# Performance work log

Hardware: AMD Instinct MI355X
Metric: run time of the kernel (lower is better)

Reference implementation:

```python
import jax, jax.numpy as jnp
import numpy as np

C = 1.0          # ball curvature (k = -1/c with c=1.0 in the torch module)
SQC = 1.0        # sqrt(C)
LN_EPS = 1e-5

def _artanh(x):
    return jnp.arctanh(jnp.clip(x, -1.0 + 1e-7, 1.0 - 1e-7))

def _norm(x):
    # last-dim L2 norm, clamped away from zero for stable division
    return jnp.clip(jnp.sqrt(jnp.sum(x * x, axis=-1, keepdims=True)), 1e-7, None)

def expmap0(u):
    un = _norm(u)
    return jnp.tanh(SQC * un) * u / (SQC * un)

def logmap0(y):
    yn = _norm(y)
    return _artanh(SQC * yn) * y / (SQC * yn)

def mobius_add(x, y):
    x2 = jnp.sum(x * x, axis=-1, keepdims=True)
    y2 = jnp.sum(y * y, axis=-1, keepdims=True)
    xy = jnp.sum(x * y, axis=-1, keepdims=True)
    num = (1.0 + 2.0 * C * xy + C * y2) * x + (1.0 - C * x2) * y
    den = 1.0 + 2.0 * C * xy + C * C * x2 * y2
    return num / jnp.clip(den, 1e-15, None)

def mobius_matvec(W, x):
    # W: [H, D], x: [B, D] -> [B, H]
    mx = x @ W.T
    xn = _norm(x)
    mxn = _norm(mx)
    res = jnp.tanh(mxn / xn * _artanh(SQC * xn)) * mx / (SQC * mxn)
    return jnp.where(mxn <= 1e-7, jnp.zeros_like(res), res)

def mobius_pointwise_mul(w, x):
    wx = w * x
    xn = _norm(x)
    wxn = _norm(wx)
    res = jnp.tanh(wxn / xn * _artanh(SQC * xn)) * wx / (SQC * wxn)
    return jnp.where(wxn <= 1e-7, jnp.zeros_like(res), res)

def layer_norm(x, g, b):
    mu = jnp.mean(x, axis=-1, keepdims=True)
    var = jnp.mean((x - mu) ** 2, axis=-1, keepdims=True)
    return (x - mu) * jax.lax.rsqrt(var + LN_EPS) * g + b

def one_rnn_transform(W, h, U, x, b):
    Wh = mobius_matvec(W, h)
    Ux = mobius_matvec(U, x)
    return mobius_add(mobius_add(Wh, Ux), b)

def setup_inputs() -> dict:
    key = jax.random.key(0)
    B, I, H = 65536, 256, 256
    k1, k2, k3, k4, k5 = jax.random.split(key, 5)
    stdv = 1.0 / np.sqrt(H)
    # points on the Poincare ball via expmap0 of small tangent vectors
    x = expmap0(0.02 * jax.random.normal(k1, (B, I), dtype=jnp.float32))
    hx = expmap0(0.02 * jax.random.normal(k2, (B, H), dtype=jnp.float32))
    weight_ih = jax.random.uniform(k3, (3 * H, I), dtype=jnp.float32, minval=-stdv, maxval=stdv)
    weight_hh = jax.random.uniform(k4, (3 * H, H), dtype=jnp.float32, minval=-stdv, maxval=stdv)
    bias = 0.01 * jax.random.normal(k5, (3, H), dtype=jnp.float32)
    ln_gamma = jnp.ones((3, H), dtype=jnp.float32)
    ln_beta = jnp.zeros((3, H), dtype=jnp.float32)
    return {"input": x, "hx": hx, "weight_ih": weight_ih, "weight_hh": weight_hh,
            "bias": bias, "ln_gamma": ln_gamma, "ln_beta": ln_beta}

def reference(input, hx, weight_ih, weight_hh, bias, ln_gamma, ln_beta):
    H = hx.shape[-1]
    W_ir, W_ih_, W_iz = weight_ih[:H], weight_ih[H:2*H], weight_ih[2*H:]
    W_hr, W_hh_, W_hz = weight_hh[:H], weight_hh[H:2*H], weight_hh[2*H:]
    b_r, b_h, b_z = bias[0], bias[1], bias[2]
    temp_z = logmap0(one_rnn_transform(W_hz, hx, W_iz, input, b_z))
    temp_r = logmap0(one_rnn_transform(W_hr, hx, W_ir, input, b_r))
    z_t = jax.nn.sigmoid(layer_norm(temp_z, ln_gamma[0], ln_beta[0]))
    r_t = jax.nn.sigmoid(layer_norm(temp_r, ln_gamma[1], ln_beta[1]))
    rh_t = mobius_pointwise_mul(r_t, hx)
    h_tilde = one_rnn_transform(W_hh_, rh_t, W_ih_, input, b_h)
    h_tilde = expmap0(jnp.tanh(layer_norm(logmap0(h_tilde), ln_gamma[2], ln_beta[2])))
    temp_1 = mobius_pointwise_mul(1.0 - z_t, hx)
    temp_2 = mobius_pointwise_mul(z_t, h_tilde)
    return mobius_add(temp_1, temp_2)
```

## Files before the change

kernel.cpp:

```cpp
#include <hip/hip_runtime.h>
#include <math.h>

#define HD  256
#define BM  16
#define NTH 256

typedef __attribute__((ext_vector_type(8))) short bf16x8;
typedef __attribute__((ext_vector_type(4))) float f32x4;

__device__ __forceinline__ float rcp_f(float x){ return __builtin_amdgcn_rcpf(x); }
__device__ __forceinline__ float tanh_f(float x){
  float ax = fabsf(x);
  float e  = __expf(-2.f*ax);
  float t  = (1.f - e) * rcp_f(1.f + e);
  return copysignf(t, x);
}
__device__ __forceinline__ float artanh_f(float v){
  v = fminf(fmaxf(v, -1.f + 1e-7f), 1.f - 1e-7f);
  return 0.5f * __logf((1.f + v) * rcp_f(1.f - v));
}
__device__ __forceinline__ float sigmoid_f(float v){ return rcp_f(1.f + __expf(-v)); }
__device__ __forceinline__ unsigned short f2bf(float f){
  unsigned u = __float_as_uint(f);
  u += 0x7FFFu + ((u >> 16) & 1u);
  return (unsigned short)(u >> 16);
}
__device__ __forceinline__ float bf2f(unsigned short h){
  return __uint_as_float(((unsigned)h) << 16);
}
__device__ __forceinline__ int swz(int R, int C){
  return R*HD + (((C >> 3) ^ (R & 7)) << 3) + (C & 7);
}

__global__ void convert_w_kernel(const float* __restrict__ Wih,
                                 const float* __restrict__ Whh,
                                 unsigned short* __restrict__ wb){
  int c = blockIdx.x * blockDim.x + threadIdx.x;
  if (c >= 6 * 8192) return;
  int mat = c >> 13;
  int ci  = c & 8191;
  int l = ci & 63, st = ci >> 6;
  int s = st & 7, ct = st >> 3;
  int col = ct * 16 + (l & 15);
  int k0  = s * 32 + (l >> 4) * 8;
  const float* src = (mat < 3) ? (Wih + (size_t)mat * HD * HD)
                               : (Whh + (size_t)(mat - 3) * HD * HD);
  const float* p = src + (size_t)col * HD + k0;
  unsigned short tmp[8];
  #pragma unroll
  for (int j = 0; j < 8; ++j) tmp[j] = f2bf(p[j]);
  *(bf16x8*)(wb + (size_t)mat * 65536 + (size_t)ci * 8) = *(bf16x8*)tmp;
}

__device__ __forceinline__ void reduce7(
    const f32x4* A, const f32x4* B, const float* bt,
    float (*RED)[33], int wc, int lr, int lg){
  float p[7][4];
  #pragma unroll
  for (int q = 0; q < 4; ++q){
    float a2=0.f,b2=0.f,ab=0.f,sA=0.f,sB=0.f,Ab=0.f,Bb=0.f;
    #pragma unroll
    for (int n = 0; n < 4; ++n){
      float ae = A[n][q], be = B[n][q], bv = bt[n];
      a2 = fmaf(ae,ae,a2); b2 = fmaf(be,be,b2); ab = fmaf(ae,be,ab);
      sA += ae; sB += be; Ab = fmaf(ae,bv,Ab); Bb = fmaf(be,bv,Bb);
    }
    p[0][q]=a2; p[1][q]=b2; p[2][q]=ab; p[3][q]=sA; p[4][q]=sB; p[5][q]=Ab; p[6][q]=Bb;
  }
  #pragma unroll
  for (int j = 0; j < 7; ++j)
    #pragma unroll
    for (int q = 0; q < 4; ++q){
      float v = p[j][q];
      v += __shfl_xor(v,1); v += __shfl_xor(v,2);
      v += __shfl_xor(v,4); v += __shfl_xor(v,8);
      p[j][q] = v;
    }
  if (lr == 0){
    #pragma unroll
    for (int q = 0; q < 4; ++q){
      int R = lg*4 + q;
      #pragma unroll
      for (int j = 0; j < 7; ++j) RED[R][wc*8 + j] = p[j][q];
    }
  }
}

__device__ __forceinline__ void chain5(
    const float* s, float bb, float sbs,
    float an, float aa, float bn, float ba, float* o){
  float mraw = sqrtf(s[0]); float mA = fmaxf(mraw, 1e-7f);
  float tA = tanh_f(mA / an * aa);
  float sa  = (mraw <= 1e-7f) ? 0.f : tA / mA;
  float x2a = (mraw <= 1e-7f) ? 0.f : tA*tA;
  float nraw = sqrtf(s[1]); float mB = fmaxf(nraw, 1e-7f);
  float tB = tanh_f(mB / bn * ba);
  float sb_ = (nraw <= 1e-7f) ? 0.f : tB / mB;
  float x2b = (nraw <= 1e-7f) ? 0.f : tB*tB;
  float xy = sa*sb_*s[2];
  float ca = 1.f + 2.f*xy + x2b;
  float cb = 1.f - x2a;
  float den = fmaxf(1.f + 2.f*xy + x2a*x2b, 1e-15f);
  float u = ca*sa/den, v = cb*sb_/den;
  float P2 = u*u*s[0] + 2.f*u*v*s[2] + v*v*s[1];
  float Pb = u*s[5] + v*s[6];
  float sP = u*s[3] + v*s[4];
  float ca2 = 1.f + 2.f*Pb + bb;
  float cb2 = 1.f - P2;
  float den2 = fmaxf(1.f + 2.f*Pb + P2*bb, 1e-15f);
  float pp = ca2/den2, ww = cb2/den2;
  float Q2 = pp*pp*P2 + 2.f*pp*ww*Pb + ww*ww*bb;
  float sQsum = pp*sP + ww*sbs;
  float qn = fmaxf(sqrtf(Q2), 1e-7f);
  float sQ = artanh_f(qn) / qn;
  float mu = sQ*sQsum*(1.f/HD);
  float e2 = sQ*sQ*Q2*(1.f/HD);
  float is = rsqrtf(e2 - mu*mu + 1e-5f);
  o[0] = sQ*pp*u;  o[1] = sQ*pp*v;  o[2] = sQ*ww;
  o[3] = mu;       o[4] = is;
}

__global__ __launch_bounds__(NTH, 2) void mobius_gru_mfma(
    const float* __restrict__ x, const float* __restrict__ hx,
    const unsigned short* __restrict__ wbih, const unsigned short* __restrict__ wbhh,
    const float* __restrict__ bias, const float* __restrict__ gam,
    const float* __restrict__ bet, float* __restrict__ out, int B){
  __shared__ unsigned short xb[BM*HD];
  __shared__ unsigned short hb[BM*HD];
  __shared__ float REDZ[BM][33];
  __shared__ float REDR[BM][33];
  __shared__ float kco[BM][10];
  __shared__ float srow[8][BM];
  __shared__ float sbb[8];

  const int t  = threadIdx.x;
  const int l  = t & 63;
  const int lr = l & 15, lg = l >> 4;
  const int wc = t >> 6;
  const size_t row0 = (size_t)blockIdx.x * BM;

  {
    float* spart = &REDZ[0][0];
    int r = t >> 4, seg = t & 15;
    const float* xp = x  + (row0 + r)*HD + seg*16;
    const float* hp = hx + (row0 + r)*HD + seg*16;
    float sx = 0.f, sh = 0.f;
    #pragma unroll
    for (int i = 0; i < 4; ++i){
      int c = seg*16 + i*4;
      int di = swz(r, c);
      float4 v = *(const float4*)(xp + i*4);
      sx += v.x*v.x + v.y*v.y + v.z*v.z + v.w*v.w;
      ushort4 o = { f2bf(v.x), f2bf(v.y), f2bf(v.z), f2bf(v.w) };
      *(ushort4*)&xb[di] = o;
      v = *(const float4*)(hp + i*4);
      sh += v.x*v.x + v.y*v.y + v.z*v.z + v.w*v.w;
      ushort4 o2 = { f2bf(v.x), f2bf(v.y), f2bf(v.z), f2bf(v.w) };
      *(ushort4*)&hb[di] = o2;
    }
    spart[r*16 + seg] = sx; spart[256 + r*16 + seg] = sh;
  }
  if (t >= 64 && t < 256){
    int g = (t >> 6) - 1;
    float4 b4 = *(const float4*)&bias[g*HD + (t & 63)*4];
    float p2 = b4.x*b4.x + b4.y*b4.y + b4.z*b4.z + b4.w*b4.w;
    float ps = b4.x + b4.y + b4.z + b4.w;
    #pragma unroll
    for (int m = 1; m <= 32; m <<= 1){ p2 += __shfl_xor(p2, m); ps += __shfl_xor(ps, m); }
    if ((t & 63) == 0){ sbb[g] = p2; sbb[4+g] = ps; }
  }
  __syncthreads();
  if (t < BM){
    float* spart = &REDZ[0][0];
    float sx = 0.f, sh = 0.f;
    #pragma unroll
    for (int i = 0; i < 16; ++i){ sx += spart[t*16 + i]; sh += spart[256 + t*16 + i]; }
    float xn = fmaxf(sqrtf(sx), 1e-7f);
    float hn = fmaxf(sqrtf(sh), 1e-7f);
    srow[0][t] = xn; srow[1][t] = artanh_f(xn);
    srow[2][t] = hn; srow[3][t] = artanh_f(hn);
  }
  __syncthreads();

  f32x4 Az[4], Bz[4], Ar[4], Br[4], Bh[4];
  float btz[4], btr[4];
  #pragma unroll
  for (int n = 0; n < 4; ++n){
    int C = wc*64 + n*16 + lr;
    btz[n] = bias[2*HD + C];
    btr[n] = bias[C];
    Az[n] = (f32x4){0.f,0.f,0.f,0.f}; Bz[n] = (f32x4){0.f,0.f,0.f,0.f};
    Ar[n] = (f32x4){0.f,0.f,0.f,0.f}; Br[n] = (f32x4){0.f,0.f,0.f,0.f};
    Bh[n] = (f32x4){0.f,0.f,0.f,0.f};
  }
  {
    const unsigned short* wHz = wbhh + 2*65536;
    const unsigned short* wXz = wbih + 2*65536;
    const unsigned short* wHr = wbhh;
    const unsigned short* wXr = wbih;
    const unsigned short* wXh = wbih + 65536;
    #pragma unroll
    for (int s = 0; s < 8; ++s){
      int idx = lr*HD + (((4*s + lg) ^ (lr & 7)) << 3);
      bf16x8 ah = *(const bf16x8*)&hb[idx];
      bf16x8 ax = *(const bf16x8*)&xb[idx];
      #pragma unroll
      for (int n = 0; n < 4; ++n){
        int off = (((wc*4 + n)*8 + s)*64 + l)*8;
        bf16x8 bhz = *(const bf16x8*)(wHz + off);
        bf16x8 bxz = *(const bf16x8*)(wXz + off);
        bf16x8 bhr = *(const bf16x8*)(wHr + off);
        bf16x8 bxr = *(const bf16x8*)(wXr + off);
        bf16x8 bxh = *(const bf16x8*)(wXh + off);
        Az[n] = __builtin_amdgcn_mfma_f32_16x16x32_bf16(ah, bhz, Az[n], 0, 0, 0);
        Bz[n] = __builtin_amdgcn_mfma_f32_16x16x32_bf16(ax, bxz, Bz[n], 0, 0, 0);
        Ar[n] = __builtin_amdgcn_mfma_f32_16x16x32_bf16(ah, bhr, Ar[n], 0, 0, 0);
        Br[n] = __builtin_amdgcn_mfma_f32_16x16x32_bf16(ax, bxr, Br[n], 0, 0, 0);
        Bh[n] = __builtin_amdgcn_mfma_f32_16x16x32_bf16(ax, bxh, Bh[n], 0, 0, 0);
      }
    }
  }
  reduce7(Az, Bz, btz, REDZ, wc, lr, lg);
  reduce7(Ar, Br, btr, REDR, wc, lr, lg);
  __syncthreads();
  if (t < 32){
    int R = t & 15, gsel = t >> 4;
    float (*REDp)[33] = gsel ? REDR : REDZ;
    int gidx = gsel ? 0 : 2;
    float s[7];
    #pragma unroll
    for (int j = 0; j < 7; ++j)
      s[j] = REDp[R][j] + REDp[R][8+j] + REDp[R][16+j] + REDp[R][24+j];
    float o[5];
    chain5(s, sbb[gidx], sbb[4+gidx],
           srow[2][R], srow[3][R], srow[0][R], srow[1][R], o);
    #pragma unroll
    for (int k = 0; k < 5; ++k) kco[R][gsel*5 + k] = o[k];
  }
  __syncthreads();

  unsigned ztp[4][2];
  float hvreg[4][4];
  {
    float gvz[4], bvz[4], gvr[4], bvr[4];
    #pragma unroll
    for (int n = 0; n < 4; ++n){
      int C = wc*64 + n*16 + lr;
      gvz[n] = gam[C];      bvz[n] = bet[C];
      gvr[n] = gam[HD + C]; bvr[n] = bet[HD + C];
    }
    #pragma unroll
    for (int q = 0; q < 4; ++q){
      int R = lg*4 + q;
      float KAz=kco[R][0], KBz=kco[R][1], Kbz=kco[R][2], muz=kco[R][3], isz=kco[R][4];
      float KAr=kco[R][5], KBr=kco[R][6], Kbr=kco[R][7], mur=kco[R][8], isr=kco[R][9];
      float acc = 0.f;
      #pragma unroll
      for (int n = 0; n < 4; ++n){
        int C = wc*64 + n*16 + lr;
        float hv = bf2f(hb[swz(R, C)]);
        hvreg[n][q] = hv;
        float lnz = (KAz*Az[n][q] + KBz*Bz[n][q] + Kbz*btz[n] - muz)*isz*gvz[n] + bvz[n];
        unsigned zb = f2bf(sigmoid_f(lnz));
        if ((q & 1) == 0) ztp[n][q>>1] = zb;
        else              ztp[n][q>>1] |= (zb << 16);
        float lnr = (KAr*Ar[n][q] + KBr*Br[n][q] + Kbr*btr[n] - mur)*isr*gvr[n] + bvr[n];
        float rhv = sigmoid_f(lnr) * hv;
        Br[n][q] = rhv;
        acc = fmaf(rhv, rhv, acc);
      }
      float v2 = acc;
      v2 += __shfl_xor(v2,1); v2 += __shfl_xor(v2,2);
      v2 += __shfl_xor(v2,4); v2 += __shfl_xor(v2,8);
      if (lr == 0) REDZ[R][wc*8] = v2;
    }
  }
  __syncthreads();
  if (t < BM){
    int R = t;
    float s0 = REDZ[R][0] + REDZ[R][8] + REDZ[R][16] + REDZ[R][24];
    float wraw = sqrtf(s0); float wn = fmaxf(wraw, 1e-7f);
    float s = tanh_f(wn / srow[2][R] * srow[3][R]);
    float sc = (wraw <= 1e-7f) ? 0.f : s / wn;
    float rn = fmaxf((wraw <= 1e-7f) ? 0.f : fabsf(s), 1e-7f);
    kco[R][0] = sc; srow[4][R] = rn; srow[5][R] = artanh_f(rn);
  }
  __syncthreads();
  #pragma unroll
  for (int q = 0; q < 4; ++q){
    int R = lg*4 + q;
    float sc = kco[R][0];
    #pragma unroll
    for (int n = 0; n < 4; ++n){
      int C = wc*64 + n*16 + lr;
      hb[swz(R, C)] = f2bf(sc * Br[n][q]);
    }
  }
  __syncthreads();

  f32x4 Ah[4];
  float bth[4];
  #pragma unroll
  for (int n = 0; n < 4; ++n){
    int C = wc*64 + n*16 + lr;
    bth[n] = bias[HD + C];
    Ah[n] = (f32x4){0.f,0.f,0.f,0.f};
  }
  {
    const unsigned short* wHh = wbhh + 65536;
    #pragma unroll
    for (int s = 0; s < 8; ++s){
      int idx = lr*HD + (((4*s + lg) ^ (lr & 7)) << 3);
      bf16x8 ar = *(const bf16x8*)&hb[idx];
      #pragma unroll
      for (int n = 0; n < 4; ++n){
        int off = (((wc*4 + n)*8 + s)*64 + l)*8;
        bf16x8 bh = *(const bf16x8*)(wHh + off);
        Ah[n] = __builtin_amdgcn_mfma_f32_16x16x32_bf16(ar, bh, Ah[n], 0, 0, 0);
      }
    }
  }
  reduce7(Ah, Bh, bth, REDZ, wc, lr, lg);
  __syncthreads();
  if (t < BM){
    int R = t;
    float s[7];
    #pragma unroll
    for (int j = 0; j < 7; ++j)
      s[j] = REDZ[R][j] + REDZ[R][8+j] + REDZ[R][16+j] + REDZ[R][24+j];
    float o[5];
    chain5(s, sbb[1], sbb[5],
           srow[4][R], srow[5][R], srow[0][R], srow[1][R], o);
    #pragma unroll
    for (int k = 0; k < 5; ++k) kco[R][k] = o[k];
  }
  __syncthreads();
  {
    float gvh[4], bvh[4];
    #pragma unroll
    for (int n = 0; n < 4; ++n){
      int C = wc*64 + n*16 + lr;
      gvh[n] = gam[2*HD + C]; bvh[n] = bet[2*HD + C];
    }
    #pragma unroll
    for (int q = 0; q < 4; ++q){
      int R = lg*4 + q;
      float KA=kco[R][0], KB=kco[R][1], Kb=kco[R][2], mu=kco[R][3], is=kco[R][4];
      float acc = 0.f;
      #pragma unroll
      for (int n = 0; n < 4; ++n){
        float ln = (KA*Ah[n][q] + KB*Bh[n][q] + Kb*bth[n] - mu)*is*gvh[n] + bvh[n];
        float uv = tanh_f(ln);
        Ah[n][q] = uv;
        acc = fmaf(uv, uv, acc);
      }
      float v2 = acc;
      v2 += __shfl_xor(v2,1); v2 += __shfl_xor(v2,2);
      v2 += __shfl_xor(v2,4); v2 += __shfl_xor(v2,8);
      if (lr == 0) REDZ[R][wc*8] = v2;
    }
  }
  __syncthreads();
  if (t < BM){
    int R = t;
    float s0 = REDZ[R][0] + REDZ[R][8] + REDZ[R][16] + REDZ[R][24];
    float unraw = sqrtf(s0);
    float un = fmaxf(unraw, 1e-7f);
    float es = tanh_f(un) / un;
    float htn = fmaxf(es * unraw, 1e-7f);
    kco[R][0] = es; srow[6][R] = htn; srow[7][R] = artanh_f(htn);
  }
  __syncthreads();

  #pragma unroll
  for (int q = 0; q < 4; ++q){
    int R = lg*4 + q;
    float es = kco[R][0];
    float a1 = 0.f, a2 = 0.f, a12 = 0.f;
    #pragma unroll
    for (int n = 0; n < 4; ++n){
      unsigned zp = ztp[n][q >> 1];
      float zv = __uint_as_float((q & 1) ? (zp & 0xFFFF0000u) : (zp << 16));
      float w2v = zv * es * Ah[n][q];
      float w1v = (1.f - zv) * hvreg[n][q];
      Ah[n][q] = w2v;
      Bh[n][q] = w1v;
      a1 = fmaf(w1v, w1v, a1); a2 = fmaf(w2v, w2v, a2); a12 = fmaf(w1v, w2v, a12);
    }
    float v1 = a1, v2 = a2, v3 = a12;
    v1 += __shfl_xor(v1,1); v2 += __shfl_xor(v2,1); v3 += __shfl_xor(v3,1);
    v1 += __shfl_xor(v1,2); v2 += __shfl_xor(v2,2); v3 += __shfl_xor(v3,2);
    v1 += __shfl_xor(v1,4); v2 += __shfl_xor(v2,4); v3 += __shfl_xor(v3,4);
    v1 += __shfl_xor(v1,8); v2 += __shfl_xor(v2,8); v3 += __shfl_xor(v3,8);
    if (lr == 0){
      REDZ[R][wc*8]   = v1;
      REDZ[R][wc*8+1] = v2;
      REDZ[R][wc*8+2] = v3;
    }
  }
  __syncthreads();
  if (t < BM){
    int R = t;
    float s1  = REDZ[R][0] + REDZ[R][8]  + REDZ[R][16] + REDZ[R][24];
    float s2  = REDZ[R][1] + REDZ[R][9]  + REDZ[R][17] + REDZ[R][25];
    float s12 = REDZ[R][2] + REDZ[R][10] + REDZ[R][18] + REDZ[R][26];
    float raw1 = sqrtf(s1); float n1 = fmaxf(raw1, 1e-7f);
    float ss1 = tanh_f(n1 / srow[2][R] * srow[3][R]);
    float sc1 = (raw1 <= 1e-7f) ? 0.f : ss1 / n1;
    float t1  = (raw1 <= 1e-7f) ? 0.f : ss1*ss1;
    float raw2 = sqrtf(s2); float n2 = fmaxf(raw2, 1e-7f);
    float ss2 = tanh_f(n2 / srow[6][R] * srow[7][R]);
    float sc2 = (raw2 <= 1e-7f) ? 0.f : ss2 / n2;
    float t2  = (raw2 <= 1e-7f) ? 0.f : ss2*ss2;
    float xy = sc1*sc2*s12;
    float ca = 1.f + 2.f*xy + t2;
    float cb = 1.f - t1;
    float den = fmaxf(1.f + 2.f*xy + t1*t2, 1e-15f);
    kco[R][0] = ca*sc1/den;
    kco[R][1] = cb*sc2/den;
  }
  __syncthreads();
  #pragma unroll
  for (int q = 0; q < 4; ++q){
    int R = lg*4 + q;
    float cw1 = kco[R][0], cw2 = kco[R][1];
    #pragma unroll
    for (int n = 0; n < 4; ++n){
      int C = wc*64 + n*16 + lr;
      out[(row0 + R)*HD + C] = cw1*Bh[n][q] + cw2*Ah[n][q];
    }
  }
}

extern "C" void kernel_launch(void* const* d_in, const int* in_sizes, int n_in,
                              void* d_out, int out_size, void* d_ws, size_t ws_size,
                              hipStream_t stream){
  const float* x    = (const float*)d_in[0];
  const float* hx   = (const float*)d_in[1];
  const float* Wih  = (const float*)d_in[2];
  const float* Whh  = (const float*)d_in[3];
  const float* bias = (const float*)d_in[4];
  const float* gam  = (const float*)d_in[5];
  const float* bet  = (const float*)d_in[6];
  float* out = (float*)d_out;
  unsigned short* wb = (unsigned short*)d_ws;
  const int B = in_sizes[0] / HD;

  hipLaunchKernelGGL(convert_w_kernel, dim3(192), dim3(256), 0, stream, Wih, Whh, wb);
  hipLaunchKernelGGL(mobius_gru_mfma, dim3(B / BM), dim3(NTH), 0, stream,
                     x, hx, wb, wb + 3*65536, bias, gam, bet, out, B);
}
```

Baseline: 219.1 us.

## Replace single-thread row epilogues with redundant per-wave compute and shuffles

Per-row scalar coefficient stages that ran on 16-32 threads, wrote to shared memory and needed an extra barrier each are now computed redundantly by every wave. Values reach the needed lanes by cross-lane shuffles, which removes several __syncthreads and the kco shared array. Reduction partials move to spare column slots so they do not collide with live data. The cost is duplicated transcendental math in every wave and more shuffle traffic.

```diff
diff --git a/kernel.cpp b/kernel.cpp
--- a/kernel.cpp
+++ b/kernel.cpp
@@ -129,7 +129,6 @@
   __shared__ unsigned short hb[BM*HD];
   __shared__ float REDZ[BM][33];
   __shared__ float REDR[BM][33];
-  __shared__ float kco[BM][10];
   __shared__ float srow[8][BM];
   __shared__ float sbb[8];
 
@@ -137,6 +136,7 @@
   const int l  = t & 63;
   const int lr = l & 15, lg = l >> 4;
   const int wc = t >> 6;
+  const int crow = lg*4 + (lr & 3);
   const size_t row0 = (size_t)blockIdx.x * BM;
 
   {
@@ -170,15 +170,15 @@
     if ((t & 63) == 0){ sbb[g] = p2; sbb[4+g] = ps; }
   }
   __syncthreads();
-  if (t < BM){
+  if (t < 32){
     float* spart = &REDZ[0][0];
-    float sx = 0.f, sh = 0.f;
-    #pragma unroll
-    for (int i = 0; i < 16; ++i){ sx += spart[t*16 + i]; sh += spart[256 + t*16 + i]; }
-    float xn = fmaxf(sqrtf(sx), 1e-7f);
-    float hn = fmaxf(sqrtf(sh), 1e-7f);
-    srow[0][t] = xn; srow[1][t] = artanh_f(xn);
-    srow[2][t] = hn; srow[3][t] = artanh_f(hn);
+    int R = t & 15, sel = t >> 4;
+    const float* base = spart + sel*256;
+    float sv = 0.f;
+    #pragma unroll
+    for (int i = 0; i < 16; ++i) sv += base[R*16 + i];
+    float nn = fmaxf(sqrtf(sv), 1e-7f);
+    srow[sel*2][R] = nn; srow[sel*2+1][R] = artanh_f(nn);
   }
   __syncthreads();
 
@@ -223,21 +223,29 @@
   reduce7(Az, Bz, btz, REDZ, wc, lr, lg);
   reduce7(Ar, Br, btr, REDR, wc, lr, lg);
   __syncthreads();
-  if (t < 32){
-    int R = t & 15, gsel = t >> 4;
-    float (*REDp)[33] = gsel ? REDR : REDZ;
-    int gidx = gsel ? 0 : 2;
+
+  float KAz[4],KBz[4],Kbz[4],muz[4],isz[4];
+  float KAr[4],KBr[4],Kbr[4],mur[4],ISr[4];
+  {
+    bool doR = (lr >= 8);
+    float (*REDp)[33] = doR ? REDR : REDZ;
+    int gidx = doR ? 0 : 2;
     float s[7];
     #pragma unroll
     for (int j = 0; j < 7; ++j)
-      s[j] = REDp[R][j] + REDp[R][8+j] + REDp[R][16+j] + REDp[R][24+j];
+      s[j] = REDp[crow][j] + REDp[crow][8+j] + REDp[crow][16+j] + REDp[crow][24+j];
     float o[5];
     chain5(s, sbb[gidx], sbb[4+gidx],
-           srow[2][R], srow[3][R], srow[0][R], srow[1][R], o);
-    #pragma unroll
-    for (int k = 0; k < 5; ++k) kco[R][gsel*5 + k] = o[k];
-  }
-  __syncthreads();
+           srow[2][crow], srow[3][crow], srow[0][crow], srow[1][crow], o);
+    #pragma unroll
+    for (int q = 0; q < 4; ++q){
+      int zs = (l & 48) + q, rs = zs + 8;
+      KAz[q]=__shfl(o[0],zs); KBz[q]=__shfl(o[1],zs); Kbz[q]=__shfl(o[2],zs);
+      muz[q]=__shfl(o[3],zs); isz[q]=__shfl(o[4],zs);
+      KAr[q]=__shfl(o[0],rs); KBr[q]=__shfl(o[1],rs); Kbr[q]=__shfl(o[2],rs);
+      mur[q]=__shfl(o[3],rs); ISr[q]=__shfl(o[4],rs);
+    }
+  }
 
   unsigned ztp[4][2];
   float hvreg[4][4];
@@ -252,19 +260,17 @@
     #pragma unroll
     for (int q = 0; q < 4; ++q){
       int R = lg*4 + q;
-      float KAz=kco[R][0], KBz=kco[R][1], Kbz=kco[R][2], muz=kco[R][3], isz=kco[R][4];
-      float KAr=kco[R][5], KBr=kco[R][6], Kbr=kco[R][7], mur=kco[R][8], isr=kco[R][9];
       float acc = 0.f;
       #pragma unroll
       for (int n = 0; n < 4; ++n){
         int C = wc*64 + n*16 + lr;
         float hv = bf2f(hb[swz(R, C)]);
         hvreg[n][q] = hv;
-        float lnz = (KAz*Az[n][q] + KBz*Bz[n][q] + Kbz*btz[n] - muz)*isz*gvz[n] + bvz[n];
+        float lnz = (KAz[q]*Az[n][q] + KBz[q]*Bz[n][q] + Kbz[q]*btz[n] - muz[q])*isz[q]*gvz[n] + bvz[n];
         unsigned zb = f2bf(sigmoid_f(lnz));
         if ((q & 1) == 0) ztp[n][q>>1] = zb;
         else              ztp[n][q>>1] |= (zb << 16);
-        float lnr = (KAr*Ar[n][q] + KBr*Br[n][q] + Kbr*btr[n] - mur)*isr*gvr[n] + bvr[n];
+        float lnr = (KAr[q]*Ar[n][q] + KBr[q]*Br[n][q] + Kbr[q]*btr[n] - mur[q])*ISr[q]*gvr[n] + bvr[n];
         float rhv = sigmoid_f(lnr) * hv;
         Br[n][q] = rhv;
         acc = fmaf(rhv, rhv, acc);
@@ -272,28 +278,29 @@
       float v2 = acc;
       v2 += __shfl_xor(v2,1); v2 += __shfl_xor(v2,2);
       v2 += __shfl_xor(v2,4); v2 += __shfl_xor(v2,8);
-      if (lr == 0) REDZ[R][wc*8] = v2;
-    }
-  }
-  __syncthreads();
-  if (t < BM){
-    int R = t;
-    float s0 = REDZ[R][0] + REDZ[R][8] + REDZ[R][16] + REDZ[R][24];
+      if (lr == 0) REDZ[R][wc*8 + 7] = v2;
+    }
+  }
+  __syncthreads();
+
+  float scq[4];
+  {
+    float s0 = REDZ[crow][7] + REDZ[crow][15] + REDZ[crow][23] + REDZ[crow][31];
     float wraw = sqrtf(s0); float wn = fmaxf(wraw, 1e-7f);
-    float s = tanh_f(wn / srow[2][R] * srow[3][R]);
-    float sc = (wraw <= 1e-7f) ? 0.f : s / wn;
-    float rn = fmaxf((wraw <= 1e-7f) ? 0.f : fabsf(s), 1e-7f);
-    kco[R][0] = sc; srow[4][R] = rn; srow[5][R] = artanh_f(rn);
-  }
-  __syncthreads();
+    float sv = tanh_f(wn / srow[2][crow] * srow[3][crow]);
+    float sc = (wraw <= 1e-7f) ? 0.f : sv / wn;
+    float rn = fmaxf((wraw <= 1e-7f) ? 0.f : fabsf(sv), 1e-7f);
+    if (wc == 0 && lr < 4){ srow[4][crow] = rn; srow[5][crow] = artanh_f(rn); }
+    #pragma unroll
+    for (int q = 0; q < 4; ++q) scq[q] = __shfl(sc, (l & 48) + q);
+  }
   #pragma unroll
   for (int q = 0; q < 4; ++q){
     int R = lg*4 + q;
-    float sc = kco[R][0];
     #pragma unroll
     for (int n = 0; n < 4; ++n){
       int C = wc*64 + n*16 + lr;
-      hb[swz(R, C)] = f2bf(sc * Br[n][q]);
+      hb[swz(R, C)] = f2bf(scq[q] * Br[n][q]);
     }
   }
   __syncthreads();
@@ -322,19 +329,23 @@
   }
   reduce7(Ah, Bh, bth, REDZ, wc, lr, lg);
   __syncthreads();
-  if (t < BM){
-    int R = t;
+
+  float KA[4],KB[4],Kb[4],MU[4],IS[4];
+  {
     float s[7];
     #pragma unroll
     for (int j = 0; j < 7; ++j)
-      s[j] = REDZ[R][j] + REDZ[R][8+j] + REDZ[R][16+j] + REDZ[R][24+j];
+      s[j] = REDZ[crow][j] + REDZ[crow][8+j] + REDZ[crow][16+j] + REDZ[crow][24+j];
     float o[5];
     chain5(s, sbb[1], sbb[5],
-           srow[4][R], srow[5][R], srow[0][R], srow[1][R], o);
-    #pragma unroll
-    for (int k = 0; k < 5; ++k) kco[R][k] = o[k];
-  }
-  __syncthreads();
+           srow[4][crow], srow[5][crow], srow[0][crow], srow[1][crow], o);
+    #pragma unroll
+    for (int q = 0; q < 4; ++q){
+      int src = (l & 48) + q;
+      KA[q]=__shfl(o[0],src); KB[q]=__shfl(o[1],src); Kb[q]=__shfl(o[2],src);
+      MU[q]=__shfl(o[3],src); IS[q]=__shfl(o[4],src);
+    }
+  }
   {
     float gvh[4], bvh[4];
     #pragma unroll
@@ -345,11 +356,10 @@
     #pragma unroll
     for (int q = 0; q < 4; ++q){
       int R = lg*4 + q;
-      float KA=kco[R][0], KB=kco[R][1], Kb=kco[R][2], mu=kco[R][3], is=kco[R][4];
       float acc = 0.f;
       #pragma unroll
       for (int n = 0; n < 4; ++n){
-        float ln = (KA*Ah[n][q] + KB*Bh[n][q] + Kb*bth[n] - mu)*is*gvh[n] + bvh[n];
+        float ln = (KA[q]*Ah[n][q] + KB[q]*Bh[n][q] + Kb[q]*bth[n] - MU[q])*IS[q]*gvh[n] + bvh[n];
         float uv = tanh_f(ln);
         Ah[n][q] = uv;
         acc = fmaf(uv, uv, acc);
@@ -357,31 +367,32 @@
       float v2 = acc;
       v2 += __shfl_xor(v2,1); v2 += __shfl_xor(v2,2);
       v2 += __shfl_xor(v2,4); v2 += __shfl_xor(v2,8);
-      if (lr == 0) REDZ[R][wc*8] = v2;
-    }
-  }
-  __syncthreads();
-  if (t < BM){
-    int R = t;
-    float s0 = REDZ[R][0] + REDZ[R][8] + REDZ[R][16] + REDZ[R][24];
+      if (lr == 0) REDZ[R][wc*8 + 7] = v2;
+    }
+  }
+  __syncthreads();
+
+  float esq[4];
+  {
+    float s0 = REDZ[crow][7] + REDZ[crow][15] + REDZ[crow][23] + REDZ[crow][31];
     float unraw = sqrtf(s0);
     float un = fmaxf(unraw, 1e-7f);
     float es = tanh_f(un) / un;
     float htn = fmaxf(es * unraw, 1e-7f);
-    kco[R][0] = es; srow[6][R] = htn; srow[7][R] = artanh_f(htn);
-  }
-  __syncthreads();
+    if (wc == 0 && lr < 4){ srow[6][crow] = htn; srow[7][crow] = artanh_f(htn); }
+    #pragma unroll
+    for (int q = 0; q < 4; ++q) esq[q] = __shfl(es, (l & 48) + q);
+  }
 
   #pragma unroll
   for (int q = 0; q < 4; ++q){
     int R = lg*4 + q;
-    float es = kco[R][0];
     float a1 = 0.f, a2 = 0.f, a12 = 0.f;
     #pragma unroll
     for (int n = 0; n < 4; ++n){
       unsigned zp = ztp[n][q >> 1];
       float zv = __uint_as_float((q & 1) ? (zp & 0xFFFF0000u) : (zp << 16));
-      float w2v = zv * es * Ah[n][q];
+      float w2v = zv * esq[q] * Ah[n][q];
       float w1v = (1.f - zv) * hvreg[n][q];
       Ah[n][q] = w2v;
       Bh[n][q] = w1v;
@@ -399,35 +410,40 @@
     }
   }
   __syncthreads();
-  if (t < BM){
-    int R = t;
-    float s1  = REDZ[R][0] + REDZ[R][8]  + REDZ[R][16] + REDZ[R][24];
-    float s2  = REDZ[R][1] + REDZ[R][9]  + REDZ[R][17] + REDZ[R][25];
-    float s12 = REDZ[R][2] + REDZ[R][10] + REDZ[R][18] + REDZ[R][26];
+
+  float cw1q[4], cw2q[4];
+  {
+    float s1  = REDZ[crow][0] + REDZ[crow][8]  + REDZ[crow][16] + REDZ[crow][24];
+    float s2  = REDZ[crow][1] + REDZ[crow][9]  + REDZ[crow][17] + REDZ[crow][25];
+    float s12 = REDZ[crow][2] + REDZ[crow][10] + REDZ[crow][18] + REDZ[crow][26];
     float raw1 = sqrtf(s1); float n1 = fmaxf(raw1, 1e-7f);
-    float ss1 = tanh_f(n1 / srow[2][R] * srow[3][R]);
+    float ss1 = tanh_f(n1 / srow[2][crow] * srow[3][crow]);
     float sc1 = (raw1 <= 1e-7f) ? 0.f : ss1 / n1;
     float t1  = (raw1 <= 1e-7f) ? 0.f : ss1*ss1;
     float raw2 = sqrtf(s2); float n2 = fmaxf(raw2, 1e-7f);
-    float ss2 = tanh_f(n2 / srow[6][R] * srow[7][R]);
+    float ss2 = tanh_f(n2 / srow[6][crow] * srow[7][crow]);
     float sc2 = (raw2 <= 1e-7f) ? 0.f : ss2 / n2;
     float t2  = (raw2 <= 1e-7f) ? 0.f : ss2*ss2;
     float xy = sc1*sc2*s12;
     float ca = 1.f + 2.f*xy + t2;
     float cb = 1.f - t1;
     float den = fmaxf(1.f + 2.f*xy + t1*t2, 1e-15f);
-    kco[R][0] = ca*sc1/den;
-    kco[R][1] = cb*sc2/den;
-  }
-  __syncthreads();
+    float cw1 = ca*sc1/den;
+    float cw2 = cb*sc2/den;
+    #pragma unroll
+    for (int q = 0; q < 4; ++q){
+      int src = (l & 48) + q;
+      cw1q[q] = __shfl(cw1, src);
+      cw2q[q] = __shfl(cw2, src);
+    }
+  }
   #pragma unroll
   for (int q = 0; q < 4; ++q){
     int R = lg*4 + q;
-    float cw1 = kco[R][0], cw2 = kco[R][1];
     #pragma unroll
     for (int n = 0; n < 4; ++n){
       int C = wc*64 + n*16 + lr;
-      out[(row0 + R)*HD + C] = cw1*Bh[n][q] + cw2*Ah[n][q];
+      out[(row0 + R)*HD + C] = cw1q[q]*Bh[n][q] + cw2q[q]*Ah[n][q];
     }
   }
 }
```

Result: slower. 247.0 us (+12.7%).
